# Kernel optimization log

Hardware: AMD Instinct MI355X
Metric: run time of the kernel (lower is better)

Reference implementation:

```python
import jax, jax.numpy as jnp
import numpy as np

LN_EPS = 1e-5

def setup_inputs() -> dict:
    key = jax.random.key(0)
    k0, k1, k2, k3 = jax.random.split(key, 4)
    B, N, D = 4, 4096, 512
    x = jax.random.normal(k0, (B, N, D), dtype=jnp.float32)
    s = 1.0 / np.sqrt(D)
    Wq = jax.random.normal(k1, (D, D), dtype=jnp.float32) * s
    Wk = jax.random.normal(k2, (D, D), dtype=jnp.float32) * s
    Wv = jax.random.normal(k3, (D, D), dtype=jnp.float32) * s
    gamma = jnp.ones((D,), dtype=jnp.float32)
    beta = jnp.zeros((D,), dtype=jnp.float32)
    return {"x": x, "Wq": Wq, "Wk": Wk, "Wv": Wv, "gamma": gamma, "beta": beta}

def reference(x, Wq, Wk, Wv, gamma, beta):
    # x: [B, N, D]
    D = x.shape[-1]
    q = jnp.einsum('bnd,de->bne', x, Wq)
    k = jnp.einsum('bnd,de->bne', x, Wk)
    v = jnp.einsum('bnd,de->bne', x, Wv)
    # full [B, N, N] score matrix, as in the original bmm chain
    dist = jnp.einsum('bne,bme->bnm', q, k) * (1.0 / jnp.sqrt(jnp.float32(D)))
    dist = jax.nn.softmax(dist, axis=-1)
    att = jnp.einsum('bnm,bmd->bnd', dist, v)
    # residual + LayerNorm over last dim
    h = att + x
    mu = jnp.mean(h, axis=-1, keepdims=True)
    var = jnp.mean(jnp.square(h - mu), axis=-1, keepdims=True)
    out = (h - mu) * jax.lax.rsqrt(var + LN_EPS) * gamma + beta
    return out
```

## Files before the change

### kernel.cpp

```cpp
#include <hip/hip_runtime.h>
#include <stdint.h>

typedef __attribute__((ext_vector_type(8))) __bf16 bf16x8;
typedef __attribute__((ext_vector_type(4))) float f32x4;
typedef __attribute__((ext_vector_type(16))) float f32x16;
typedef unsigned short u16;
typedef unsigned char u8;
typedef unsigned int u32;
typedef long i64;

#define LN_EPS 1e-5f

__device__ __forceinline__ float bf2f(u16 u){
  union { u32 i; float f; } v; v.i = ((u32)u) << 16; return v.f;
}
__device__ __forceinline__ u16 f2bf(float f){
  union { float f; u32 i; } v; v.f = f;
  u32 u = v.i;
  u += 0x7fffu + ((u >> 16) & 1u);
  return (u16)(u >> 16);
}
__device__ __forceinline__ u8 f2fp8(float f){
  union { float f; u32 i; } v; v.f = f;
  u32 s = (v.i >> 24) & 0x80u;
  u32 u = v.i & 0x7FFFFFFFu;
  if (u < 0x3C800000u) return (u8)s;
  if (u > 0x43E00000u) u = 0x43E00000u;
  u += 0x7FFFFu + ((u >> 20) & 1u);
  int e = (int)(u >> 23) - 120;
  u32 m = (u >> 20) & 7u;
  return (u8)(s | ((u32)e << 3) | m);
}

__device__ __forceinline__ void gload_lds16(const void* g, void* l) {
  __builtin_amdgcn_global_load_lds(
      (const __attribute__((address_space(1))) void*)g,
      (__attribute__((address_space(3))) void*)l, 16, 0, 0);
}

__global__ void xcast_kernel(const float* __restrict__ X, u16* __restrict__ Xb) {
  int idx = (blockIdx.x * 256 + threadIdx.x) * 8;
  float4 f0 = *(const float4*)&X[idx];
  float4 f1 = *(const float4*)&X[idx + 4];
  ushort4 lo, hi;
  lo.x = f2bf(f0.x); lo.y = f2bf(f0.y); lo.z = f2bf(f0.z); lo.w = f2bf(f0.w);
  hi.x = f2bf(f1.x); hi.y = f2bf(f1.y); hi.z = f2bf(f1.z); hi.w = f2bf(f1.w);
  *(ushort4*)&Xb[idx] = lo;
  *(ushort4*)&Xb[idx + 4] = hi;
}

__global__ void transpose_w_kernel(const float* __restrict__ Wq,
                                   const float* __restrict__ Wk,
                                   const float* __restrict__ Wv,
                                   u16* __restrict__ Wt) {
  const float* W = (blockIdx.y == 0) ? Wq : ((blockIdx.y == 1) ? Wk : Wv);
  u16* o = Wt + blockIdx.y * 512 * 512;
  int idx = blockIdx.x * 256 + threadIdx.x;
  int e = idx >> 9, d = idx & 511;
  o[e * 512 + d] = f2bf(W[d * 512 + e]);
}

__launch_bounds__(256, 4)
__global__ void qkv_gemm_kernel(const u16* __restrict__ Xb,
                                const u16* __restrict__ Wt,
                                u8* __restrict__ Qo,
                                u8* __restrict__ Ko,
                                u8* __restrict__ Vto8) {
  const int z = blockIdx.y;
  const u16* Wtm = Wt + z * 512 * 512;
  const int mblk = blockIdx.x & 127;
  const int nblk = blockIdx.x >> 7;
  const int m0 = mblk * 128, n0 = nblk * 128;

  __shared__ __align__(16) u8 As[128 * 64];
  __shared__ __align__(16) u8 Bs[128 * 64];

  const int tid = threadIdx.x;
  const int lane = tid & 63, w = tid >> 6;
  const int wr = w >> 1, wc = w & 1;
  const int lrow = lane & 15, quad = lane >> 4;

  f32x4 acc[4][4];
#pragma unroll
  for (int i = 0; i < 4; i++)
#pragma unroll
    for (int j = 0; j < 4; j++) acc[i][j] = (f32x4){0.f, 0.f, 0.f, 0.f};

  const int srow = lane >> 2;
  const int spos = lane & 3;

#pragma unroll
  for (int r2 = 0; r2 < 2; r2++) {
    int rowb = w * 32 + r2 * 16;
    int row = rowb + srow;
    int g = spos ^ (row & 3);
    gload_lds16(&Xb[(m0 + row) * 512 + g * 8], &As[rowb * 64]);
    gload_lds16(&Wtm[(n0 + row) * 512 + g * 8], &Bs[rowb * 64]);
  }

  for (int k = 0; k < 16; k++) {
    __syncthreads();
    bf16x8 a[4], b[4];
#pragma unroll
    for (int t = 0; t < 4; t++) {
      int ra = wr * 64 + t * 16 + lrow;
      a[t] = *(const bf16x8*)&As[ra * 64 + (quad ^ (ra & 3)) * 16];
      int rb = wc * 64 + t * 16 + lrow;
      b[t] = *(const bf16x8*)&Bs[rb * 64 + (quad ^ (rb & 3)) * 16];
    }
    __syncthreads();
    if (k < 15) {
      int k0n = (k + 1) * 32;
#pragma unroll
      for (int r2 = 0; r2 < 2; r2++) {
        int rowb = w * 32 + r2 * 16;
        int row = rowb + srow;
        int g = spos ^ (row & 3);
        gload_lds16(&Xb[(m0 + row) * 512 + k0n + g * 8], &As[rowb * 64]);
        gload_lds16(&Wtm[(n0 + row) * 512 + k0n + g * 8], &Bs[rowb * 64]);
      }
    }
#pragma unroll
    for (int i = 0; i < 4; i++)
#pragma unroll
      for (int j = 0; j < 4; j++)
        acc[i][j] = __builtin_amdgcn_mfma_f32_16x16x32_bf16(a[i], b[j], acc[i][j], 0, 0, 0);
  }

  if (z < 2) {
    u8* O = (z == 0) ? Qo : Ko;
#pragma unroll
    for (int i = 0; i < 4; i++) {
      int rbase = m0 + wr * 64 + i * 16 + quad * 4;
#pragma unroll
      for (int j = 0; j < 4; j++) {
        int col = n0 + wc * 64 + j * 16 + lrow;
#pragma unroll
        for (int r = 0; r < 4; r++)
          O[(rbase + r) * 512 + col] = f2fp8(acc[i][j][r]);
      }
    }
  } else {
#pragma unroll
    for (int i = 0; i < 4; i++) {
      int rbase = m0 + wr * 64 + i * 16 + quad * 4;
#pragma unroll
      for (int j = 0; j < 4; j++) {
        int col = n0 + wc * 64 + j * 16 + lrow;
        uchar4 pk;
        pk.x = f2fp8(acc[i][j][0]);
        pk.y = f2fp8(acc[i][j][1]);
        pk.z = f2fp8(acc[i][j][2]);
        pk.w = f2fp8(acc[i][j][3]);
        *(uchar4*)&Vto8[col * 16384 + rbase] = pk;
      }
    }
  }
}

__launch_bounds__(256, 2)
__global__ void attn_partial_kernel(const u8* __restrict__ Q,
                                    const u8* __restrict__ K,
                                    const u8* __restrict__ Vt8,
                                    u16* __restrict__ O0b,
                                    u16* __restrict__ O1b,
                                    float* __restrict__ L) {
  const int b = blockIdx.y;
  const int split = blockIdx.z;
  const int q0 = blockIdx.x * 64;
  const int tid = threadIdx.x;
  const int lane = tid & 63, w = tid >> 6;
  const int lrow = lane & 15, quad = lane >> 4;
  const int l31 = lane & 31, half = lane >> 5;

  __shared__ __align__(16) u8 Ks8[32 * 512];
  __shared__ __align__(16) u8 Vs8[512 * 32];
  __shared__ __align__(16) u8 Pb8[64 * 40];

  const int keybase = b * 4096 + split * 2048;

  const int qtok = b * 4096 + q0 + w * 16 + lrow;
  i64 qf[16];
#pragma unroll
  for (int s = 0; s < 16; s++)
    qf[s] = *(const i64*)&Q[qtok * 512 + s * 32 + quad * 8];

  f32x16 Oacc[2][4];
#pragma unroll
  for (int i = 0; i < 2; i++)
#pragma unroll
    for (int j = 0; j < 4; j++)
#pragma unroll
      for (int e = 0; e < 16; e++) Oacc[i][j][e] = 0.f;

  float lsum[4] = {0.f, 0.f, 0.f, 0.f};
  const float scale = 0.044194173824159216f;

#pragma unroll
  for (int i = 0; i < 4; i++) {
    int row = w * 8 + i * 2 + (lane >> 5);
    int g = (lane & 31) ^ (row & 7);
    gload_lds16(&K[(keybase + row) * 512 + g * 16], &Ks8[(w * 8 + i * 2) * 512]);
  }
#pragma unroll
  for (int run = 0; run < 4; run++) {
    int rowb = w * 128 + run * 32;
    int n = rowb + (lane >> 1);
    int g16 = (lane & 1) ^ ((n >> 2) & 1);
    gload_lds16(&Vt8[n * 16384 + keybase + g16 * 16], &Vs8[rowb * 32]);
  }

  for (int it = 0; it < 64; ++it) {
    __syncthreads();

    f32x4 S0 = {0.f, 0.f, 0.f, 0.f}, S1 = {0.f, 0.f, 0.f, 0.f};
#pragma unroll
    for (int s = 0; s < 16; s++) {
      int gs = (2 * s + (quad >> 1)) ^ (lrow & 7);
      int off = gs * 16 + (quad & 1) * 8;
      i64 k0 = *(const i64*)&Ks8[lrow * 512 + off];
      i64 k1 = *(const i64*)&Ks8[(16 + lrow) * 512 + off];
      S0 = __builtin_amdgcn_mfma_f32_16x16x32_fp8_fp8(qf[s], k0, S0, 0, 0, 0);
      S1 = __builtin_amdgcn_mfma_f32_16x16x32_fp8_fp8(qf[s], k1, S1, 0, 0, 0);
    }

#pragma unroll
    for (int r = 0; r < 4; r++) {
      float p0 = __expf(S0[r] * scale);
      float p1 = __expf(S1[r] * scale);
      lsum[r] += p0 + p1;
      int prow = w * 16 + quad * 4 + r;
      Pb8[prow * 40 + lrow] = f2fp8(p0);
      Pb8[prow * 40 + 16 + lrow] = f2fp8(p1);
    }

    __syncthreads();

    const int kknext = (it + 1) * 32;
    if (it < 63) {
#pragma unroll
      for (int i = 0; i < 4; i++) {
        int row = w * 8 + i * 2 + (lane >> 5);
        int g = (lane & 31) ^ (row & 7);
        gload_lds16(&K[(keybase + kknext + row) * 512 + g * 16],
                    &Ks8[(w * 8 + i * 2) * 512]);
      }
    }

    i64 af[2][2];
#pragma unroll
    for (int i = 0; i < 2; i++)
#pragma unroll
      for (int kg = 0; kg < 2; kg++)
        af[i][kg] = *(const i64*)&Pb8[(i * 32 + l31) * 40 + kg * 16 + half * 8];

    i64 bv[4][2];
#pragma unroll
    for (int j = 0; j < 4; j++) {
      int n = w * 128 + j * 32 + l31;
      int x = (n >> 2) & 1;
#pragma unroll
      for (int kg = 0; kg < 2; kg++)
        bv[j][kg] = *(const i64*)&Vs8[n * 32 + (kg ^ x) * 16 + half * 8];
    }

    asm volatile("s_waitcnt lgkmcnt(0)" ::: "memory");

    if (it < 63) {
#pragma unroll
      for (int run = 0; run < 4; run++) {
        int rowb = w * 128 + run * 32;
        int n = rowb + (lane >> 1);
        int g16 = (lane & 1) ^ ((n >> 2) & 1);
        gload_lds16(&Vt8[n * 16384 + keybase + kknext + g16 * 16], &Vs8[rowb * 32]);
      }
    }

#pragma unroll
    for (int j = 0; j < 4; j++)
#pragma unroll
      for (int i = 0; i < 2; i++) {
        Oacc[i][j] = __builtin_amdgcn_mfma_f32_32x32x16_fp8_fp8(af[i][0], bv[j][0], Oacc[i][j], 0, 0, 0);
        Oacc[i][j] = __builtin_amdgcn_mfma_f32_32x32x16_fp8_fp8(af[i][1], bv[j][1], Oacc[i][j], 0, 0, 0);
      }
  }

#pragma unroll
  for (int r = 0; r < 4; r++) {
    float s = lsum[r];
    s += __shfl_xor(s, 1); s += __shfl_xor(s, 2);
    s += __shfl_xor(s, 4); s += __shfl_xor(s, 8);
    lsum[r] = s;
  }
  const int tokw = b * 4096 + q0 + w * 16 + quad * 4;
  if (lrow == 0) {
#pragma unroll
    for (int r = 0; r < 4; r++)
      L[split * 16384 + tokw + r] = lsum[r];
  }

  u16* Ob = (split == 0) ? O0b : O1b;
  const int tokbase = b * 4096 + q0;
#pragma unroll
  for (int i = 0; i < 2; i++)
#pragma unroll
    for (int j = 0; j < 4; j++) {
      int col = w * 128 + j * 32 + l31;
#pragma unroll
      for (int p = 0; p < 16; p++) {
        int row = i * 32 + (p & 3) + 8 * (p >> 2) + 4 * half;
        Ob[(tokbase + row) * 512 + col] = f2bf(Oacc[i][j][p]);
      }
    }
}

__launch_bounds__(256)
__global__ void combine_ln_kernel(const u16* __restrict__ O0b,
                                  const u16* __restrict__ O1b,
                                  const float* __restrict__ L,
                                  const float* __restrict__ X,
                                  const float* __restrict__ gamma,
                                  const float* __restrict__ beta,
                                  float* __restrict__ Out) {
  const int lane = threadIdx.x & 63;
  const int tok = blockIdx.x * 4 + (threadIdx.x >> 6);
  const float inv_l = 1.f / (L[tok] + L[16384 + tok]);
  const int base = tok * 512 + lane * 8;

  uint4 avec = *(const uint4*)&O0b[base];
  uint4 bvec = *(const uint4*)&O1b[base];
  const u16* ap = (const u16*)&avec;
  const u16* bp = (const u16*)&bvec;
  float4 x0 = *(const float4*)&X[base];
  float4 x1 = *(const float4*)&X[base + 4];
  const float* xp = (const float*)&x0;
  float xs[8] = {x0.x, x0.y, x0.z, x0.w, x1.x, x1.y, x1.z, x1.w};
  (void)xp;

  float h[8];
#pragma unroll
  for (int i = 0; i < 8; i++)
    h[i] = (bf2f(ap[i]) + bf2f(bp[i])) * inv_l + xs[i];

  float sum = 0.f, sq = 0.f;
#pragma unroll
  for (int i = 0; i < 8; i++) { sum += h[i]; sq += h[i] * h[i]; }
#pragma unroll
  for (int d = 1; d < 64; d <<= 1) {
    sum += __shfl_xor(sum, d);
    sq  += __shfl_xor(sq, d);
  }
  float mu = sum * (1.f / 512.f);
  float var = sq * (1.f / 512.f) - mu * mu;
  float rstd = rsqrtf(var + LN_EPS);

  float4 g0 = *(const float4*)&gamma[lane * 8];
  float4 g1 = *(const float4*)&gamma[lane * 8 + 4];
  float4 b0 = *(const float4*)&beta[lane * 8];
  float4 b1 = *(const float4*)&beta[lane * 8 + 4];
  float gs[8] = {g0.x, g0.y, g0.z, g0.w, g1.x, g1.y, g1.z, g1.w};
  float bs[8] = {b0.x, b0.y, b0.z, b0.w, b1.x, b1.y, b1.z, b1.w};

  float4 o0, o1;
  float* op = (float*)&o0;
#pragma unroll
  for (int i = 0; i < 4; i++) op[i] = (h[i] - mu) * rstd * gs[i] + bs[i];
  float* op1 = (float*)&o1;
#pragma unroll
  for (int i = 0; i < 4; i++) op1[i] = (h[i + 4] - mu) * rstd * gs[i + 4] + bs[i + 4];
  *(float4*)&Out[base] = o0;
  *(float4*)&Out[base + 4] = o1;
}

extern "C" void kernel_launch(void* const* d_in, const int* in_sizes, int n_in,
                              void* d_out, int out_size, void* d_ws, size_t ws_size,
                              hipStream_t stream) {
  const float* x = (const float*)d_in[0];
  const float* Wq = (const float*)d_in[1];
  const float* Wk = (const float*)d_in[2];
  const float* Wv = (const float*)d_in[3];
  const float* gamma = (const float*)d_in[4];
  const float* beta = (const float*)d_in[5];

  char* ws = (char*)d_ws;
  u8*  Qws   = (u8*)(ws);
  u8*  Kws   = (u8*)(ws + 8388608);
  u8*  Vt8ws = (u8*)(ws + 16777216);
  u16* Wtws  = (u16*)(ws + 25165824);
  u16* Xbws  = (u16*)(ws + 26738688);
  u16* O0bws = (u16*)(ws + 26738688);
  u16* O1bws = (u16*)(ws + 43515904);
  float* Lws = (float*)(ws + 60293120);

  hipLaunchKernelGGL(xcast_kernel, dim3(4096), dim3(256), 0, stream, x, Xbws);
  hipLaunchKernelGGL(transpose_w_kernel, dim3(1024, 3), dim3(256), 0, stream,
                     Wq, Wk, Wv, Wtws);
  hipLaunchKernelGGL(qkv_gemm_kernel, dim3(512, 3), dim3(256), 0, stream,
                     Xbws, Wtws, Qws, Kws, Vt8ws);
  hipLaunchKernelGGL(attn_partial_kernel, dim3(64, 4, 2), dim3(256), 0, stream,
                     Qws, Kws, Vt8ws, O0bws, O1bws, Lws);
  hipLaunchKernelGGL(combine_ln_kernel, dim3(4096), dim3(256), 0, stream,
                     O0bws, O1bws, Lws, x, gamma, beta, (float*)d_out);
}
```

Baseline: 275.3 us.

## Double-buffer K/V tiles in attention and use hardware FP8 pack conversion

```diff
diff --git a/kernel.cpp b/kernel.cpp
--- a/kernel.cpp
+++ b/kernel.cpp
@@ -20,16 +20,10 @@
   u += 0x7fffu + ((u >> 16) & 1u);
   return (u16)(u >> 16);
 }
-__device__ __forceinline__ u8 f2fp8(float f){
-  union { float f; u32 i; } v; v.f = f;
-  u32 s = (v.i >> 24) & 0x80u;
-  u32 u = v.i & 0x7FFFFFFFu;
-  if (u < 0x3C800000u) return (u8)s;
-  if (u > 0x43E00000u) u = 0x43E00000u;
-  u += 0x7FFFFu + ((u >> 20) & 1u);
-  int e = (int)(u >> 23) - 120;
-  u32 m = (u >> 20) & 7u;
-  return (u8)(s | ((u32)e << 3) | m);
+__device__ __forceinline__ u32 cvt_pk_fp8(float a, float b){
+  u32 pk;
+  asm("v_cvt_pk_fp8_f32 %0, %1, %2" : "=v"(pk) : "v"(a), "v"(b));
+  return pk;
 }
 
 __device__ __forceinline__ void gload_lds16(const void* g, void* l) {
@@ -135,9 +129,12 @@
 #pragma unroll
       for (int j = 0; j < 4; j++) {
         int col = n0 + wc * 64 + j * 16 + lrow;
-#pragma unroll
-        for (int r = 0; r < 4; r++)
-          O[(rbase + r) * 512 + col] = f2fp8(acc[i][j][r]);
+        u32 pk01 = cvt_pk_fp8(acc[i][j][0], acc[i][j][1]);
+        u32 pk23 = cvt_pk_fp8(acc[i][j][2], acc[i][j][3]);
+        O[(rbase + 0) * 512 + col] = (u8)pk01;
+        O[(rbase + 1) * 512 + col] = (u8)(pk01 >> 8);
+        O[(rbase + 2) * 512 + col] = (u8)pk23;
+        O[(rbase + 3) * 512 + col] = (u8)(pk23 >> 8);
       }
     }
   } else {
@@ -147,12 +144,10 @@
 #pragma unroll
       for (int j = 0; j < 4; j++) {
         int col = n0 + wc * 64 + j * 16 + lrow;
-        uchar4 pk;
-        pk.x = f2fp8(acc[i][j][0]);
-        pk.y = f2fp8(acc[i][j][1]);
-        pk.z = f2fp8(acc[i][j][2]);
-        pk.w = f2fp8(acc[i][j][3]);
-        *(uchar4*)&Vto8[col * 16384 + rbase] = pk;
+        u32 pk01 = cvt_pk_fp8(acc[i][j][0], acc[i][j][1]);
+        u32 pk23 = cvt_pk_fp8(acc[i][j][2], acc[i][j][3]);
+        u32 pk = (pk01 & 0xffffu) | (pk23 << 16);
+        *(u32*)&Vto8[col * 16384 + rbase] = pk;
       }
     }
   }
@@ -173,8 +168,8 @@
   const int lrow = lane & 15, quad = lane >> 4;
   const int l31 = lane & 31, half = lane >> 5;
 
-  __shared__ __align__(16) u8 Ks8[32 * 512];
-  __shared__ __align__(16) u8 Vs8[512 * 32];
+  __shared__ __align__(16) u8 Ks8[2][32 * 512];
+  __shared__ __align__(16) u8 Vs8[2][512 * 32];
   __shared__ __align__(16) u8 Pb8[64 * 40];
 
   const int keybase = b * 4096 + split * 2048;
@@ -184,6 +179,9 @@
 #pragma unroll
   for (int s = 0; s < 16; s++)
     qf[s] = *(const i64*)&Q[qtok * 512 + s * 32 + quad * 8];
+#pragma unroll
+  for (int s = 0; s < 16; s++)
+    asm volatile("" : "+v"(qf[s]));
 
   f32x16 Oacc[2][4];
 #pragma unroll
@@ -196,56 +194,66 @@
   float lsum[4] = {0.f, 0.f, 0.f, 0.f};
   const float scale = 0.044194173824159216f;
 
-#pragma unroll
-  for (int i = 0; i < 4; i++) {
-    int row = w * 8 + i * 2 + (lane >> 5);
-    int g = (lane & 31) ^ (row & 7);
-    gload_lds16(&K[(keybase + row) * 512 + g * 16], &Ks8[(w * 8 + i * 2) * 512]);
-  }
-#pragma unroll
-  for (int run = 0; run < 4; run++) {
-    int rowb = w * 128 + run * 32;
-    int n = rowb + (lane >> 1);
-    int g16 = (lane & 1) ^ ((n >> 2) & 1);
-    gload_lds16(&Vt8[n * 16384 + keybase + g16 * 16], &Vs8[rowb * 32]);
-  }
+  auto stageK = [&](int kk, u8* Kbuf) {
+#pragma unroll
+    for (int i = 0; i < 4; i++) {
+      int row = w * 8 + i * 2 + (lane >> 5);
+      int g = (lane & 31) ^ (row & 7);
+      gload_lds16(&K[(keybase + kk + row) * 512 + g * 16],
+                  &Kbuf[(w * 8 + i * 2) * 512]);
+    }
+  };
+  auto stageV = [&](int kk, u8* Vbuf) {
+#pragma unroll
+    for (int run = 0; run < 4; run++) {
+      int rowb = w * 128 + run * 32;
+      int n = rowb + (lane >> 1);
+      int g16 = (lane & 1) ^ ((n >> 2) & 1);
+      gload_lds16(&Vt8[n * 16384 + keybase + kk + g16 * 16], &Vbuf[rowb * 32]);
+    }
+  };
+
+  stageK(0, Ks8[0]);  stageV(0, Vs8[0]);
+  stageK(32, Ks8[1]); stageV(32, Vs8[1]);
 
   for (int it = 0; it < 64; ++it) {
-    __syncthreads();
+    const int cur = it & 1;
+    u8* Ksc = Ks8[cur];
+    u8* Vsc = Vs8[cur];
+
+    if (it == 63) { asm volatile("s_waitcnt vmcnt(0)" ::: "memory"); }
+    else         { asm volatile("s_waitcnt vmcnt(8)" ::: "memory"); }
+    __builtin_amdgcn_s_barrier();
 
     f32x4 S0 = {0.f, 0.f, 0.f, 0.f}, S1 = {0.f, 0.f, 0.f, 0.f};
+    __builtin_amdgcn_s_setprio(1);
 #pragma unroll
     for (int s = 0; s < 16; s++) {
       int gs = (2 * s + (quad >> 1)) ^ (lrow & 7);
       int off = gs * 16 + (quad & 1) * 8;
-      i64 k0 = *(const i64*)&Ks8[lrow * 512 + off];
-      i64 k1 = *(const i64*)&Ks8[(16 + lrow) * 512 + off];
+      i64 k0 = *(const i64*)&Ksc[lrow * 512 + off];
+      i64 k1 = *(const i64*)&Ksc[(16 + lrow) * 512 + off];
       S0 = __builtin_amdgcn_mfma_f32_16x16x32_fp8_fp8(qf[s], k0, S0, 0, 0, 0);
       S1 = __builtin_amdgcn_mfma_f32_16x16x32_fp8_fp8(qf[s], k1, S1, 0, 0, 0);
     }
+    __builtin_amdgcn_s_setprio(0);
 
 #pragma unroll
     for (int r = 0; r < 4; r++) {
       float p0 = __expf(S0[r] * scale);
       float p1 = __expf(S1[r] * scale);
       lsum[r] += p0 + p1;
+      u32 pk = cvt_pk_fp8(p0, p1);
       int prow = w * 16 + quad * 4 + r;
-      Pb8[prow * 40 + lrow] = f2fp8(p0);
-      Pb8[prow * 40 + 16 + lrow] = f2fp8(p1);
-    }
-
-    __syncthreads();
-
-    const int kknext = (it + 1) * 32;
-    if (it < 63) {
-#pragma unroll
-      for (int i = 0; i < 4; i++) {
-        int row = w * 8 + i * 2 + (lane >> 5);
-        int g = (lane & 31) ^ (row & 7);
-        gload_lds16(&K[(keybase + kknext + row) * 512 + g * 16],
-                    &Ks8[(w * 8 + i * 2) * 512]);
-      }
-    }
+      Pb8[prow * 40 + lrow] = (u8)pk;
+      Pb8[prow * 40 + 16 + lrow] = (u8)(pk >> 8);
+    }
+
+    asm volatile("s_waitcnt lgkmcnt(0)" ::: "memory");
+    __builtin_amdgcn_s_barrier();
+
+    const int kk2 = (it + 2) * 32;
+    if (kk2 < 2048) stageK(kk2, Ksc);
 
     i64 af[2][2];
 #pragma unroll
@@ -261,21 +269,14 @@
       int x = (n >> 2) & 1;
 #pragma unroll
       for (int kg = 0; kg < 2; kg++)
-        bv[j][kg] = *(const i64*)&Vs8[n * 32 + (kg ^ x) * 16 + half * 8];
+        bv[j][kg] = *(const i64*)&Vsc[n * 32 + (kg ^ x) * 16 + half * 8];
     }
 
     asm volatile("s_waitcnt lgkmcnt(0)" ::: "memory");
 
-    if (it < 63) {
-#pragma unroll
-      for (int run = 0; run < 4; run++) {
-        int rowb = w * 128 + run * 32;
-        int n = rowb + (lane >> 1);
-        int g16 = (lane & 1) ^ ((n >> 2) & 1);
-        gload_lds16(&Vt8[n * 16384 + keybase + kknext + g16 * 16], &Vs8[rowb * 32]);
-      }
-    }
-
+    if (kk2 < 2048) stageV(kk2, Vsc);
+
+    __builtin_amdgcn_s_setprio(1);
 #pragma unroll
     for (int j = 0; j < 4; j++)
 #pragma unroll
@@ -283,6 +284,7 @@
         Oacc[i][j] = __builtin_amdgcn_mfma_f32_32x32x16_fp8_fp8(af[i][0], bv[j][0], Oacc[i][j], 0, 0, 0);
         Oacc[i][j] = __builtin_amdgcn_mfma_f32_32x32x16_fp8_fp8(af[i][1], bv[j][1], Oacc[i][j], 0, 0, 0);
       }
+    __builtin_amdgcn_s_setprio(0);
   }
 
 #pragma unroll
@@ -333,9 +335,7 @@
   const u16* bp = (const u16*)&bvec;
   float4 x0 = *(const float4*)&X[base];
   float4 x1 = *(const float4*)&X[base + 4];
-  const float* xp = (const float*)&x0;
   float xs[8] = {x0.x, x0.y, x0.z, x0.w, x1.x, x1.y, x1.z, x1.w};
-  (void)xp;
 
   float h[8];
 #pragma unroll
```

Measured after the change: 296.9 us. +7.9%, slower.
